# Kernel optimization log

Hardware: AMD Instinct MI355X
Metric: run time of the kernel (lower is better)

## Reference

```python
import jax, jax.numpy as jnp
import numpy as np

B, T, C, H = 4, 2048, 1024, 16
D = C // H  # head_dim = 64

def setup_inputs() -> dict:
    key = jax.random.key(0)
    k1, k2, k3 = jax.random.split(key, 3)
    x = jax.random.normal(k1, (B, T, C), dtype=jnp.float32)
    # Linear weights stored as (out_features, in_features) like torch; we apply x @ W.T
    w_attn = jax.random.normal(k2, (3 * C, C), dtype=jnp.float32) * (1.0 / np.sqrt(C))
    w_proj = jax.random.normal(k3, (C, C), dtype=jnp.float32) * (1.0 / np.sqrt(C))
    return {"x": x, "w_attn": w_attn, "w_proj": w_proj}

def reference(x, w_attn, w_proj):
    Bv, Tv, Cv = x.shape
    qkv = jnp.einsum('btc,fc->btf', x, w_attn)  # [B,T,3C]
    q, k, v = jnp.split(qkv, 3, axis=-1)
    # [B,H,T,D]
    q = q.reshape(Bv, Tv, H, D).transpose(0, 2, 1, 3)
    k = k.reshape(Bv, Tv, H, D).transpose(0, 2, 1, 3)
    v = v.reshape(Bv, Tv, H, D).transpose(0, 2, 1, 3)
    scale = 1.0 / np.sqrt(D).astype(np.float32)
    att = jnp.einsum('bhqd,bhkd->bhqk', q, k) * scale
    causal = jnp.tril(jnp.ones((Tv, Tv), dtype=bool))
    att = jnp.where(causal, att, -jnp.inf)
    att = jax.nn.softmax(att, axis=-1)
    y = jnp.einsum('bhqk,bhkd->bhqd', att, v)
    y = y.transpose(0, 2, 1, 3).reshape(Bv, Tv, Cv)
    return jnp.einsum('btc,oc->bto', y, w_proj)
```

## Files before the change

### kernel.cpp

```cpp
#include <hip/hip_runtime.h>
#include <cstdint>
#include <cstddef>

typedef __attribute__((ext_vector_type(8))) short short8;
typedef __attribute__((ext_vector_type(4))) float f32x4;
typedef unsigned int u32;

#define MFMA_BF16(a, b, c) __builtin_amdgcn_mfma_f32_16x16x32_bf16((a), (b), (c), 0, 0, 0)

__device__ __forceinline__ void async16(const void* g, void* l) {
  __builtin_amdgcn_global_load_lds(
      (const __attribute__((address_space(1))) u32*)g,
      (__attribute__((address_space(3))) u32*)l, 16, 0, 0);
}

__device__ __forceinline__ short f2bf(float f) {
  u32 u = __builtin_bit_cast(u32, f);
  u += 0x7fffu + ((u >> 16) & 1u);
  return (short)(u >> 16);
}

__device__ __forceinline__ u32 pack_bf16_trunc(float lo, float hi) {
  return __builtin_amdgcn_perm(__builtin_bit_cast(u32, hi),
                               __builtin_bit_cast(u32, lo), 0x07060302u);
}

__global__ __launch_bounds__(256) void cast_all_kernel(
    const float* __restrict__ x, const float* __restrict__ wa,
    const float* __restrict__ wp, short* __restrict__ xb,
    short* __restrict__ wab, short* __restrict__ wpb) {
  const int i = blockIdx.x * blockDim.x + threadIdx.x;
  const float4* src;
  short4* dst;
  float sc = 1.0f;
  if (i < 2097152) {
    src = (const float4*)x + i;
    dst = (short4*)xb + i;
  } else if (i < 2883584) {
    const int j = i - 2097152;
    if (j < 262144) sc = 0.18033688011112042f;
    src = (const float4*)wa + j;
    dst = (short4*)wab + j;
  } else {
    const int j = i - 2883584;
    src = (const float4*)wp + j;
    dst = (short4*)wpb + j;
  }
  float4 v = *src;
  short4 r;
  r.x = f2bf(v.x * sc); r.y = f2bf(v.y * sc);
  r.z = f2bf(v.z * sc); r.w = f2bf(v.w * sc);
  *dst = r;
}

template <bool OUT_BF16>
__global__ __launch_bounds__(256) void gemm_bt_kernel(
    const short* __restrict__ A, const short* __restrict__ Bt,
    void* __restrict__ Cv, int M, int N, int K) {
  __shared__ __align__(16) short As[128 * 64];
  __shared__ __align__(16) short Bs[128 * 64];

  const int tid  = threadIdx.x;
  const int lane = tid & 63;
  const int wave = tid >> 6;
  const int quad = lane >> 4;
  const int l15  = lane & 15;

  const int id  = blockIdx.y * gridDim.x + blockIdx.x;
  const int xcd = id & 7;
  const int j   = id >> 3;
  const int by  = xcd * 8 + (j & 7);
  const int bx  = j >> 3;
  const int bm  = by * 128;
  const int bn  = bx * 128;

  const int wm = (wave >> 1) * 64;
  const int wn = (wave & 1) * 64;

  f32x4 acc[4][4];
#pragma unroll
  for (int i = 0; i < 4; ++i)
#pragma unroll
    for (int jj = 0; jj < 4; ++jj) acc[i][jj] = (f32x4){0.f, 0.f, 0.f, 0.f};

  int srow[4], scol[4];
#pragma unroll
  for (int it = 0; it < 4; ++it) {
    const int s = tid + it * 256;
    srow[it] = s >> 3;
    scol[it] = ((s & 7) ^ (srow[it] & 7)) * 8;
  }
  const int xk = l15 & 7;

  for (int k0 = 0; k0 < K; k0 += 64) {
    __syncthreads();
#pragma unroll
    for (int it = 0; it < 4; ++it) {
      const int s = tid + it * 256;
      async16(A  + (size_t)(bm + srow[it]) * K + k0 + scol[it], &As[s * 8]);
      async16(Bt + (size_t)(bn + srow[it]) * K + k0 + scol[it], &Bs[s * 8]);
    }
    __syncthreads();

    short8 af[4][2], bf[4][2];
#pragma unroll
    for (int mt = 0; mt < 4; ++mt) {
      const int ra = (wm + mt * 16 + l15) * 64;
      af[mt][0] = *(const short8*)&As[ra + ((quad) ^ xk) * 8];
      af[mt][1] = *(const short8*)&As[ra + ((4 + quad) ^ xk) * 8];
    }
#pragma unroll
    for (int nt = 0; nt < 4; ++nt) {
      const int rb = (wn + nt * 16 + l15) * 64;
      bf[nt][0] = *(const short8*)&Bs[rb + ((quad) ^ xk) * 8];
      bf[nt][1] = *(const short8*)&Bs[rb + ((4 + quad) ^ xk) * 8];
    }
#pragma unroll
    for (int kk = 0; kk < 2; ++kk)
#pragma unroll
      for (int mt = 0; mt < 4; ++mt)
#pragma unroll
        for (int nt = 0; nt < 4; ++nt)
          acc[mt][nt] = MFMA_BF16(af[mt][kk], bf[nt][kk], acc[mt][nt]);
  }

#pragma unroll
  for (int mt = 0; mt < 4; ++mt) {
    const int r0e = bm + wm + mt * 16 + quad * 4;
#pragma unroll
    for (int nt = 0; nt < 4; ++nt) {
      const int c = bn + wn + nt * 16 + l15;
#pragma unroll
      for (int reg = 0; reg < 4; ++reg) {
        float v = acc[mt][nt][reg];
        if (OUT_BF16)
          ((short*)Cv)[(size_t)(r0e + reg) * N + c] = f2bf(v);
        else
          ((float*)Cv)[(size_t)(r0e + reg) * N + c] = v;
      }
    }
  }
}

__global__ __launch_bounds__(256) void vtrans_kernel(
    const short* __restrict__ qkv, short* __restrict__ vt) {
  __shared__ __align__(16) short Ts[64 * 80];
  const int t0 = blockIdx.x * 64;
  const int bh = blockIdx.y;
  const int b = bh >> 4, h = bh & 15;
  const int tid = threadIdx.x;
#pragma unroll
  for (int it = 0; it < 2; ++it) {
    const int ci = tid + it * 256;
    const int t = ci >> 3, cw = ci & 7;
    short8 v = *(const short8*)(qkv + (size_t)(b * 2048 + t0 + t) * 3072 +
                                2048 + h * 64 + cw * 8);
    *(short8*)&Ts[t * 80 + cw * 8] = v;
  }
  __syncthreads();
#pragma unroll
  for (int it = 0; it < 2; ++it) {
    const int ci = tid + it * 256;
    const int d = ci >> 3, c2 = ci & 7;
    short tmp[8];
#pragma unroll
    for (int j = 0; j < 8; ++j) tmp[j] = Ts[(c2 * 8 + j) * 80 + d];
    *(short8*)(vt + (size_t)(bh * 64 + d) * 2048 + t0 + c2 * 8) =
        *(short8*)tmp;
  }
}

__global__ __launch_bounds__(256, 2) void attn_kernel(
    const short* __restrict__ qkv, const short* __restrict__ vt,
    short* __restrict__ y) {
  __shared__ __align__(16) short Ks[2][4096];
  __shared__ __align__(16) short Vs[2][4096];
  __shared__ __align__(16) short Ps[4][1024];

  const int bh    = blockIdx.x;
  const int pairi = blockIdx.y;
  const int b = bh >> 4, h = bh & 15;
  const int tid  = threadIdx.x;
  const int lane = tid & 63;
  const int wave = tid >> 6;
  const int quad = lane >> 4, l15 = lane & 15;
  const int base_row = b * 2048;
  short* Pw = &Ps[wave][0];

  const int s0 = tid, s1 = tid + 256;
  const int r0s = s0 >> 3, c0s = (s0 & 7) ^ (r0s & 7);
  const int r1s = s1 >> 3, c1s = (s1 & 7) ^ (r1s & 7);
  const short* kbase0 = qkv + (size_t)(base_row + r0s) * 3072 + 1024 + h * 64 + c0s * 8;
  const short* kbase1 = qkv + (size_t)(base_row + r1s) * 3072 + 1024 + h * 64 + c1s * 8;
  const short* vbase0 = vt + (size_t)(bh * 64 + r0s) * 2048 + c0s * 8;
  const short* vbase1 = vt + (size_t)(bh * 64 + r1s) * 2048 + c1s * 8;

  const int xk = l15 & 7;

  for (int half = 0; half < 2; ++half) {
    const int qi  = half ? (15 - pairi) : pairi;
    const int r0  = qi * 128;
    const int nkt = 2 * qi + 2;
    const int qg0a = r0 + wave * 32;

    short8 qf[2][2];
#pragma unroll
    for (int g = 0; g < 2; ++g) {
      const short* qp = qkv +
          (size_t)(base_row + qg0a + g * 16 + l15) * 3072 + h * 64 + quad * 8;
      qf[g][0] = *(const short8*)qp;
      qf[g][1] = *(const short8*)(qp + 32);
    }
    float l_r[2] = {0.f, 0.f};
    f32x4 o[2][4];
#pragma unroll
    for (int g = 0; g < 2; ++g)
#pragma unroll
      for (int dt = 0; dt < 4; ++dt) o[g][dt] = (f32x4){0.f, 0.f, 0.f, 0.f};

    async16(kbase0, &Ks[0][s0 * 8]);
    async16(kbase1, &Ks[0][s1 * 8]);
    async16(vbase0, &Vs[0][s0 * 8]);
    async16(vbase1, &Vs[0][s1 * 8]);

    for (int kt = 0; kt < nkt; ++kt) {
      const int kvb = kt * 64;
      __syncthreads();

      if (kt + 1 < nkt) {
        const int nb = (kt + 1) & 1;
        const size_t koff = (size_t)(kvb + 64) * 3072;
        async16(kbase0 + koff, &Ks[nb][s0 * 8]);
        async16(kbase1 + koff, &Ks[nb][s1 * 8]);
        async16(vbase0 + kvb + 64, &Vs[nb][s0 * 8]);
        async16(vbase1 + kvb + 64, &Vs[nb][s1 * 8]);
      }
      const short* Kb = &Ks[kt & 1][0];
      const short* Vb = &Vs[kt & 1][0];

      short8 kf[4][2];
#pragma unroll
      for (int nt = 0; nt < 4; ++nt) {
        kf[nt][0] = *(const short8*)&Kb[(nt * 16 + l15) * 64 + ((quad) ^ xk) * 8];
        kf[nt][1] = *(const short8*)&Kb[(nt * 16 + l15) * 64 + ((4 + quad) ^ xk) * 8];
      }
      short8 vf[4][2];
#pragma unroll
      for (int dt = 0; dt < 4; ++dt) {
        vf[dt][0] = *(const short8*)&Vb[(dt * 16 + l15) * 64 + ((quad) ^ xk) * 8];
        vf[dt][1] = *(const short8*)&Vb[(dt * 16 + l15) * 64 + ((4 + quad) ^ xk) * 8];
      }

#pragma unroll
      for (int g = 0; g < 2; ++g) {
        const int qg0 = qg0a + g * 16;
        if (kvb > qg0 + 15) continue;

        f32x4 s[4];
#pragma unroll
        for (int nt = 0; nt < 4; ++nt) {
          s[nt] = MFMA_BF16(kf[nt][0], qf[g][0], ((f32x4){0.f, 0.f, 0.f, 0.f}));
          s[nt] = MFMA_BF16(kf[nt][1], qf[g][1], s[nt]);
        }

        float p[4][4];
        if (kvb + 64 <= qg0) {
#pragma unroll
          for (int nt = 0; nt < 4; ++nt)
#pragma unroll
            for (int r = 0; r < 4; ++r)
              p[nt][r] = __builtin_amdgcn_exp2f(s[nt][r]);
        } else {
          const int qrel = qg0 + l15 - kvb;
#pragma unroll
          for (int nt = 0; nt < 4; ++nt)
#pragma unroll
            for (int r = 0; r < 4; ++r) {
              const int kvl = nt * 16 + quad * 4 + r;
              p[nt][r] = (kvl <= qrel) ? __builtin_amdgcn_exp2f(s[nt][r]) : 0.f;
            }
        }

        float rs = ((p[0][0] + p[0][1]) + (p[0][2] + p[0][3])) +
                   ((p[1][0] + p[1][1]) + (p[1][2] + p[1][3])) +
                   ((p[2][0] + p[2][1]) + (p[2][2] + p[2][3])) +
                   ((p[3][0] + p[3][1]) + (p[3][2] + p[3][3]));
        rs += __shfl_xor(rs, 16);
        rs += __shfl_xor(rs, 32);
        l_r[g] += rs;

#pragma unroll
        for (int nt = 0; nt < 4; ++nt) {
          u32 w0 = pack_bf16_trunc(p[nt][0], p[nt][1]);
          u32 w1 = pack_bf16_trunc(p[nt][2], p[nt][3]);
          const int p0 = 8 * nt + 2 * quad;
          u32* dst = (u32*)Pw + (p0 >> 4) * 256 + ((p0 >> 2) & 3) * 64 +
                     l15 * 4 + (p0 & 3);
          *(uint2*)dst = make_uint2(w0, w1);
        }
        short8 pf0 = *(const short8*)&Pw[quad * 128 + l15 * 8];
        short8 pf1 = *(const short8*)&Pw[512 + quad * 128 + l15 * 8];

#pragma unroll
        for (int dt = 0; dt < 4; ++dt) {
          o[g][dt] = MFMA_BF16(vf[dt][0], pf0, o[g][dt]);
          o[g][dt] = MFMA_BF16(vf[dt][1], pf1, o[g][dt]);
        }
      }
    }

#pragma unroll
    for (int g = 0; g < 2; ++g) {
      const float inv = 1.f / l_r[g];
#pragma unroll
      for (int dt = 0; dt < 4; ++dt) {
        const int d = dt * 16 + quad * 4;
        u32 w0 = pack_bf16_trunc(o[g][dt][0] * inv, o[g][dt][1] * inv);
        u32 w1 = pack_bf16_trunc(o[g][dt][2] * inv, o[g][dt][3] * inv);
        *(uint2*)&Pw[(d >> 5) * 512 + l15 * 32 + (d & 31)] = make_uint2(w0, w1);
      }
      const int qq = lane >> 2, ck = lane & 3;
      const size_t yrow = (size_t)(base_row + qg0a + g * 16 + qq);
#pragma unroll
      for (int kkd = 0; kkd < 2; ++kkd) {
        short8 vv = *(const short8*)&Pw[kkd * 512 + qq * 32 + ck * 8];
        *(short8*)(y + yrow * 1024 + h * 64 + kkd * 32 + ck * 8) = vv;
      }
    }
    __syncthreads();
  }
}

extern "C" void kernel_launch(void* const* d_in, const int* in_sizes, int n_in,
                              void* d_out, int out_size, void* d_ws,
                              size_t ws_size, hipStream_t stream) {
  const float* x  = (const float*)d_in[0];
  const float* wa = (const float*)d_in[1];
  const float* wp = (const float*)d_in[2];
  float* out = (float*)d_out;

  char* ws = (char*)d_ws;
  short* xb  = (short*)(ws + 0);
  short* wab = (short*)(ws + 16777216);
  short* wpb = (short*)(ws + 23068672);
  short* qkv = (short*)(ws + 25165824);
  short* yb  = (short*)(ws + 75497472);
  short* vtb = xb;

  cast_all_kernel<<<12288, 256, 0, stream>>>(x, wa, wp, xb, wab, wpb);

  gemm_bt_kernel<true><<<dim3(3072 / 128, 8192 / 128), 256, 0, stream>>>(
      xb, wab, (void*)qkv, 8192, 3072, 1024);

  vtrans_kernel<<<dim3(32, 64), 256, 0, stream>>>(qkv, vtb);

  attn_kernel<<<dim3(64, 8), 256, 0, stream>>>(qkv, vtb, yb);

  gemm_bt_kernel<false><<<dim3(1024 / 128, 8192 / 128), 256, 0, stream>>>(
      yb, wpb, (void*)out, 8192, 1024, 1024);
}
```

Before: 243.3 us.

## Shrink attention query tile to 64 rows and double grid with higher occupancy

The attention kernel now gives each block 64 query rows (16 per wave) instead of 128, keeping the paired causal scheduling over 32 query tiles, and doubles the grid's y dimension. Launch bounds ask for 4 blocks per CU instead of 2, since per-thread state is halved. The aim is more concurrent blocks and better latency hiding over 1024 blocks. The cost is that each K/V tile loaded into LDS is reused by half as many query rows, so K/V traffic per unit of work doubles.

New measurement: 247.6 us. About the same (+1.8%).

```diff
diff --git a/kernel.cpp b/kernel.cpp
--- a/kernel.cpp
+++ b/kernel.cpp
@@ -170,7 +170,7 @@
   }
 }
 
-__global__ __launch_bounds__(256, 2) void attn_kernel(
+__global__ __launch_bounds__(256, 4) void attn_kernel(
     const short* __restrict__ qkv, const short* __restrict__ vt,
     short* __restrict__ y) {
   __shared__ __align__(16) short Ks[2][4096];
@@ -198,25 +198,21 @@
   const int xk = l15 & 7;
 
   for (int half = 0; half < 2; ++half) {
-    const int qi  = half ? (15 - pairi) : pairi;
-    const int r0  = qi * 128;
-    const int nkt = 2 * qi + 2;
-    const int qg0a = r0 + wave * 32;
-
-    short8 qf[2][2];
-#pragma unroll
-    for (int g = 0; g < 2; ++g) {
+    const int qi  = half ? (31 - pairi) : pairi;
+    const int nkt = qi + 1;
+    const int qg0 = qi * 64 + wave * 16;
+
+    short8 qf[2];
+    {
       const short* qp = qkv +
-          (size_t)(base_row + qg0a + g * 16 + l15) * 3072 + h * 64 + quad * 8;
-      qf[g][0] = *(const short8*)qp;
-      qf[g][1] = *(const short8*)(qp + 32);
-    }
-    float l_r[2] = {0.f, 0.f};
-    f32x4 o[2][4];
-#pragma unroll
-    for (int g = 0; g < 2; ++g)
-#pragma unroll
-      for (int dt = 0; dt < 4; ++dt) o[g][dt] = (f32x4){0.f, 0.f, 0.f, 0.f};
+          (size_t)(base_row + qg0 + l15) * 3072 + h * 64 + quad * 8;
+      qf[0] = *(const short8*)qp;
+      qf[1] = *(const short8*)(qp + 32);
+    }
+    float l_r = 0.f;
+    f32x4 o[4];
+#pragma unroll
+    for (int dt = 0; dt < 4; ++dt) o[dt] = (f32x4){0.f, 0.f, 0.f, 0.f};
 
     async16(kbase0, &Ks[0][s0 * 8]);
     async16(kbase1, &Ks[0][s1 * 8]);
@@ -251,76 +247,69 @@
         vf[dt][1] = *(const short8*)&Vb[(dt * 16 + l15) * 64 + ((4 + quad) ^ xk) * 8];
       }
 
-#pragma unroll
-      for (int g = 0; g < 2; ++g) {
-        const int qg0 = qg0a + g * 16;
-        if (kvb > qg0 + 15) continue;
-
-        f32x4 s[4];
-#pragma unroll
-        for (int nt = 0; nt < 4; ++nt) {
-          s[nt] = MFMA_BF16(kf[nt][0], qf[g][0], ((f32x4){0.f, 0.f, 0.f, 0.f}));
-          s[nt] = MFMA_BF16(kf[nt][1], qf[g][1], s[nt]);
-        }
-
-        float p[4][4];
-        if (kvb + 64 <= qg0) {
-#pragma unroll
-          for (int nt = 0; nt < 4; ++nt)
-#pragma unroll
-            for (int r = 0; r < 4; ++r)
-              p[nt][r] = __builtin_amdgcn_exp2f(s[nt][r]);
-        } else {
-          const int qrel = qg0 + l15 - kvb;
-#pragma unroll
-          for (int nt = 0; nt < 4; ++nt)
-#pragma unroll
-            for (int r = 0; r < 4; ++r) {
-              const int kvl = nt * 16 + quad * 4 + r;
-              p[nt][r] = (kvl <= qrel) ? __builtin_amdgcn_exp2f(s[nt][r]) : 0.f;
-            }
-        }
-
-        float rs = ((p[0][0] + p[0][1]) + (p[0][2] + p[0][3])) +
-                   ((p[1][0] + p[1][1]) + (p[1][2] + p[1][3])) +
-                   ((p[2][0] + p[2][1]) + (p[2][2] + p[2][3])) +
-                   ((p[3][0] + p[3][1]) + (p[3][2] + p[3][3]));
-        rs += __shfl_xor(rs, 16);
-        rs += __shfl_xor(rs, 32);
-        l_r[g] += rs;
-
-#pragma unroll
-        for (int nt = 0; nt < 4; ++nt) {
-          u32 w0 = pack_bf16_trunc(p[nt][0], p[nt][1]);
-          u32 w1 = pack_bf16_trunc(p[nt][2], p[nt][3]);
-          const int p0 = 8 * nt + 2 * quad;
-          u32* dst = (u32*)Pw + (p0 >> 4) * 256 + ((p0 >> 2) & 3) * 64 +
-                     l15 * 4 + (p0 & 3);
-          *(uint2*)dst = make_uint2(w0, w1);
-        }
-        short8 pf0 = *(const short8*)&Pw[quad * 128 + l15 * 8];
-        short8 pf1 = *(const short8*)&Pw[512 + quad * 128 + l15 * 8];
-
-#pragma unroll
-        for (int dt = 0; dt < 4; ++dt) {
-          o[g][dt] = MFMA_BF16(vf[dt][0], pf0, o[g][dt]);
-          o[g][dt] = MFMA_BF16(vf[dt][1], pf1, o[g][dt]);
-        }
-      }
-    }
-
-#pragma unroll
-    for (int g = 0; g < 2; ++g) {
-      const float inv = 1.f / l_r[g];
+      f32x4 s[4];
+#pragma unroll
+      for (int nt = 0; nt < 4; ++nt) {
+        s[nt] = MFMA_BF16(kf[nt][0], qf[0], ((f32x4){0.f, 0.f, 0.f, 0.f}));
+        s[nt] = MFMA_BF16(kf[nt][1], qf[1], s[nt]);
+      }
+
+      float p[4][4];
+      if (kvb + 64 <= qg0) {
+#pragma unroll
+        for (int nt = 0; nt < 4; ++nt)
+#pragma unroll
+          for (int r = 0; r < 4; ++r)
+            p[nt][r] = __builtin_amdgcn_exp2f(s[nt][r]);
+      } else {
+        const int qrel = qg0 + l15 - kvb;
+#pragma unroll
+        for (int nt = 0; nt < 4; ++nt)
+#pragma unroll
+          for (int r = 0; r < 4; ++r) {
+            const int kvl = nt * 16 + quad * 4 + r;
+            p[nt][r] = (kvl <= qrel) ? __builtin_amdgcn_exp2f(s[nt][r]) : 0.f;
+          }
+      }
+
+      float rs = ((p[0][0] + p[0][1]) + (p[0][2] + p[0][3])) +
+                 ((p[1][0] + p[1][1]) + (p[1][2] + p[1][3])) +
+                 ((p[2][0] + p[2][1]) + (p[2][2] + p[2][3])) +
+                 ((p[3][0] + p[3][1]) + (p[3][2] + p[3][3]));
+      rs += __shfl_xor(rs, 16);
+      rs += __shfl_xor(rs, 32);
+      l_r += rs;
+
+#pragma unroll
+      for (int nt = 0; nt < 4; ++nt) {
+        u32 w0 = pack_bf16_trunc(p[nt][0], p[nt][1]);
+        u32 w1 = pack_bf16_trunc(p[nt][2], p[nt][3]);
+        const int p0 = 8 * nt + 2 * quad;
+        u32* dst = (u32*)Pw + (p0 >> 4) * 256 + ((p0 >> 2) & 3) * 64 +
+                   l15 * 4 + (p0 & 3);
+        *(uint2*)dst = make_uint2(w0, w1);
+      }
+      short8 pf0 = *(const short8*)&Pw[quad * 128 + l15 * 8];
+      short8 pf1 = *(const short8*)&Pw[512 + quad * 128 + l15 * 8];
+
+#pragma unroll
+      for (int dt = 0; dt < 4; ++dt) {
+        o[dt] = MFMA_BF16(vf[dt][0], pf0, o[dt]);
+        o[dt] = MFMA_BF16(vf[dt][1], pf1, o[dt]);
+      }
+    }
+
+    {
+      const float inv = 1.f / l_r;
 #pragma unroll
       for (int dt = 0; dt < 4; ++dt) {
         const int d = dt * 16 + quad * 4;
-        u32 w0 = pack_bf16_trunc(o[g][dt][0] * inv, o[g][dt][1] * inv);
-        u32 w1 = pack_bf16_trunc(o[g][dt][2] * inv, o[g][dt][3] * inv);
+        u32 w0 = pack_bf16_trunc(o[dt][0] * inv, o[dt][1] * inv);
+        u32 w1 = pack_bf16_trunc(o[dt][2] * inv, o[dt][3] * inv);
         *(uint2*)&Pw[(d >> 5) * 512 + l15 * 32 + (d & 31)] = make_uint2(w0, w1);
       }
       const int qq = lane >> 2, ck = lane & 3;
-      const size_t yrow = (size_t)(base_row + qg0a + g * 16 + qq);
+      const size_t yrow = (size_t)(base_row + qg0 + qq);
 #pragma unroll
       for (int kkd = 0; kkd < 2; ++kkd) {
         short8 vv = *(const short8*)&Pw[kkd * 512 + qq * 32 + ck * 8];
@@ -354,7 +343,7 @@
 
   vtrans_kernel<<<dim3(32, 64), 256, 0, stream>>>(qkv, vtb);
 
-  attn_kernel<<<dim3(64, 8), 256, 0, stream>>>(qkv, vtb, yb);
+  attn_kernel<<<dim3(64, 16), 256, 0, stream>>>(qkv, vtb, yb);
 
   gemm_bt_kernel<false><<<dim3(1024 / 128, 8192 / 128), 256, 0, stream>>>(
       yb, wpb, (void*)out, 8192, 1024, 1024);
```
